# Kernel tuning notes

Measured on AMD Instinct MI355X. Metric: run time of the kernel, lower is better.

Reference implementation:

```python
import jax, jax.numpy as jnp
from jax import lax
import numpy as np

D_MODEL, D_INNER, D_STATE, DT_RANK, D_CONV = 1024, 2048, 16, 64, 4
BATCH, SEQ = 2, 1024
EPS = 1e-5


def setup_inputs() -> dict:
    key = jax.random.key(0)
    ks = jax.random.split(key, 10)
    s_in = 1.0 / np.sqrt(D_MODEL)
    s_x = 1.0 / np.sqrt(D_INNER)
    s_dt = DT_RANK ** -0.5
    # dt_proj bias init as in the source: inv-softplus of dt ~ logU(1e-3, 1e-1)
    dt = jnp.exp(jax.random.uniform(ks[7], (D_INNER,)) * (np.log(0.1) - np.log(0.001)) + np.log(0.001))
    dt = jnp.clip(dt, 1e-4, None)
    inv_dt = dt + jnp.log(-jnp.expm1(-dt))
    A_log = jnp.log(jnp.broadcast_to(jnp.arange(1, D_STATE + 1, dtype=jnp.float32), (D_INNER, D_STATE)))
    return {
        "u": jax.random.normal(ks[0], (BATCH, SEQ, D_MODEL), jnp.float32),
        "w_norm": jnp.ones((D_MODEL,), jnp.float32),
        "w_in": jax.random.normal(ks[1], (2 * D_INNER, D_MODEL), jnp.float32) * s_in,
        "conv_w": jax.random.normal(ks[2], (D_INNER, 1, D_CONV), jnp.float32) * 0.5,
        "conv_b": jax.random.normal(ks[3], (D_INNER,), jnp.float32) * 0.1,
        "w_x": jax.random.normal(ks[4], (DT_RANK + 2 * D_STATE, D_INNER), jnp.float32) * s_x,
        "w_dt": jax.random.uniform(ks[5], (D_INNER, DT_RANK), jnp.float32, -s_dt, s_dt),
        "b_dt": inv_dt,
        "A_log": A_log,
        "D_param": jnp.ones((D_INNER,), jnp.float32),
        "w_out": jax.random.normal(ks[6], (D_MODEL, D_INNER), jnp.float32) * s_x,
    }


def reference(u, w_norm, w_in, conv_w, conv_b, w_x, w_dt, b_dt, A_log, D_param, w_out):
    d_inner, d_state = A_log.shape
    dt_rank = w_dt.shape[1]
    # RMSNorm
    rms = jnp.sqrt(jnp.mean(u * u, axis=-1, keepdims=True) + EPS)
    u_norm = w_norm * (u / rms)
    # in_proj -> split x, z
    xz = jnp.einsum('bld,ed->ble', u_norm, w_in)
    x, z = jnp.split(xz, 2, axis=-1)
    # causal depthwise conv1d (left pad d_conv-1 == torch pad+truncate)
    xt = x.transpose(0, 2, 1)  # (B, D, L)
    conv = lax.conv_general_dilated(
        xt, conv_w, window_strides=(1,), padding=[(conv_w.shape[-1] - 1, 0)],
        feature_group_count=d_inner, dimension_numbers=('NCH', 'OIH', 'NCH'))
    x = jax.nn.silu((conv + conv_b[None, :, None]).transpose(0, 2, 1))  # (B, L, D)
    # x_proj -> dt, B, C
    xp = jnp.einsum('bld,ed->ble', x, w_x)
    dt_r = xp[..., :dt_rank]
    Bm = xp[..., dt_rank:dt_rank + d_state]   # (B, L, N)
    Cm = xp[..., dt_rank + d_state:]          # (B, L, N)
    dt = jax.nn.softplus(jnp.einsum('blr,dr->bld', dt_r, w_dt) + b_dt)
    # discretize
    A = -jnp.exp(A_log)                        # (D, N)
    dA = jnp.exp(dt[..., None] * A)            # (B, L, D, N)
    dBu = dt[..., None] * Bm[:, :, None, :] * x[..., None]  # (B, L, D, N)
    # sequential selective scan over L via lax.scan
    def step(s, inp):
        dA_t, dBu_t, C_t = inp
        s = dA_t * s + dBu_t                   # (B, D, N)
        y_t = jnp.einsum('bdn,bn->bd', s, C_t)
        return s, y_t
    s0 = jnp.zeros((u.shape[0], d_inner, d_state), x.dtype)
    _, ys = lax.scan(step, s0, (dA.transpose(1, 0, 2, 3), dBu.transpose(1, 0, 2, 3), Cm.transpose(1, 0, 2)))
    y = ys.transpose(1, 0, 2) + x * D_param    # (B, L, D)
    # gate + out_proj + residual
    y = y * jax.nn.silu(z)
    return jnp.einsum('bld,ed->ble', y, w_out) + u
```

## Files before the change

### kernel.cpp

```cpp
#include <hip/hip_runtime.h>
#include <hip/hip_bf16.h>
#include <cstdint>
#include <cstddef>

#define D_MODEL 1024
#define D_INNER 2048
#define D_STATE 16
#define DT_RANK 64
#define D_CONV  4
#define BATCH   2
#define SEQ     1024
#define NTOK    (BATCH*SEQ)
#define NC      32
#define CHUNK   (SEQ/NC)

typedef __bf16 bf16;
typedef __attribute__((ext_vector_type(8))) __bf16 bf16x8;
typedef __attribute__((ext_vector_type(4))) float f32x4;

#define WS_UNORM   0
#define WS_WIN     (WS_UNORM + 4194304)
#define WS_WOUT    (WS_WIN + 8388608)
#define WS_WDT     (WS_WOUT + 4194304)
#define WS_WX      (WS_WDT + 262144)
#define WS_DTR     (WS_WX + 524288)
#define WS_XZ      (WS_DTR + 262144)
#define WS_XC      (WS_XZ + 33554432)
#define WS_XCB     (WS_XC + 16777216)
#define WS_XP      (WS_XCB + 8388608)
#define WS_DT      (WS_XP + 1048576)
#define WS_P       (WS_DT + 16777216)
#define WS_Q       (WS_P + 8388608)
#define WS_S       (WS_Q + 8388608)
#define WS_YB      (WS_S + 8388608)

__device__ __forceinline__ void gload16(const void* gsrc, void* ldst) {
    __builtin_amdgcn_global_load_lds(
        (const __attribute__((address_space(1))) unsigned int*)gsrc,
        (__attribute__((address_space(3))) unsigned int*)ldst,
        16, 0, 0);
}

__global__ void mamba_cvt4(const float* __restrict__ s, bf16* __restrict__ d, int n4) {
    int i = blockIdx.x * 256 + threadIdx.x;
    if (i < n4) {
        float4 v = ((const float4*)s)[i];
        bf16* o = d + i * 4;
        o[0] = (bf16)v.x; o[1] = (bf16)v.y; o[2] = (bf16)v.z; o[3] = (bf16)v.w;
    }
}

__global__ void mamba_cvt_pad4(const float* __restrict__ s, bf16* __restrict__ d,
                               int nsrc4, int ntot4) {
    int i = blockIdx.x * 256 + threadIdx.x;
    if (i < ntot4) {
        bf16* o = d + i * 4;
        if (i < nsrc4) {
            float4 v = ((const float4*)s)[i];
            o[0] = (bf16)v.x; o[1] = (bf16)v.y; o[2] = (bf16)v.z; o[3] = (bf16)v.w;
        } else {
            o[0] = (bf16)0.f; o[1] = (bf16)0.f; o[2] = (bf16)0.f; o[3] = (bf16)0.f;
        }
    }
}

__global__ void mamba_dtr(const float* __restrict__ xp, bf16* __restrict__ dtr) {
    int i = blockIdx.x * 256 + threadIdx.x;
    int t = i >> 4, r4 = (i & 15) * 4;
    float4 v = *(const float4*)&xp[t * 128 + r4];
    bf16* o = dtr + t * 64 + r4;
    o[0] = (bf16)v.x; o[1] = (bf16)v.y; o[2] = (bf16)v.z; o[3] = (bf16)v.w;
}

__global__ void mamba_rmsnorm(const float* __restrict__ u, const float* __restrict__ w,
                              bf16* __restrict__ out) {
    int t = blockIdx.x;
    int tid = threadIdx.x;
    const float4 v = ((const float4*)(u + (size_t)t * D_MODEL))[tid];
    float ss = v.x * v.x + v.y * v.y + v.z * v.z + v.w * v.w;
    #pragma unroll
    for (int off = 32; off; off >>= 1) ss += __shfl_xor(ss, off, 64);
    __shared__ float red[4];
    int lane = tid & 63, wv = tid >> 6;
    if (lane == 0) red[wv] = ss;
    __syncthreads();
    float tot = red[0] + red[1] + red[2] + red[3];
    float rinv = rsqrtf(tot * (1.0f / D_MODEL) + 1e-5f);
    const float4 wn = ((const float4*)w)[tid];
    bf16* op = out + (size_t)t * D_MODEL + tid * 4;
    op[0] = (bf16)(v.x * wn.x * rinv);
    op[1] = (bf16)(v.y * wn.y * rinv);
    op[2] = (bf16)(v.z * wn.z * rinv);
    op[3] = (bf16)(v.w * wn.w * rinv);
}

template <int EPI, int SPLITK>
__global__ __launch_bounds__(256)
void mamba_gemm(const bf16* __restrict__ A, const bf16* __restrict__ B, float* __restrict__ C,
                int M, int N, int K, const float* __restrict__ aux) {
    __shared__ __align__(16) bf16 As[128 * 64];
    __shared__ __align__(16) bf16 Bs[128 * 64];
    int tid = threadIdx.x;
    int lane = tid & 63, w = tid >> 6;
    int wr = w >> 1, wc = w & 1;
    int m0 = blockIdx.y * 128, n0 = blockIdx.x * 128;
    int r16 = lane & 15, kq = lane >> 4;

    int Kc = K / SPLITK;
    int kbeg = blockIdx.z * Kc;
    int kend = kbeg + Kc;

    f32x4 acc[4][4];
    #pragma unroll
    for (int i = 0; i < 4; ++i)
        #pragma unroll
        for (int j = 0; j < 4; ++j)
            acc[i][j] = (f32x4){0.f, 0.f, 0.f, 0.f};

    int srow = tid >> 3;
    int p    = tid & 7;

    for (int k0 = kbeg; k0 < kend; k0 += 64) {
        __syncthreads();
        #pragma unroll
        for (int s = 0; s < 4; ++s) {
            int row = s * 32 + srow;
            int q = p ^ (row & 7);
            gload16(A + (size_t)(m0 + row) * K + k0 + q * 8,
                    (char*)As + s * 4096 + w * 1024);
            gload16(B + (size_t)(n0 + row) * K + k0 + q * 8,
                    (char*)Bs + s * 4096 + w * 1024);
        }
        __syncthreads();
        #pragma unroll
        for (int sub = 0; sub < 2; ++sub) {
            bf16x8 af[4], bfr[4];
            #pragma unroll
            for (int i = 0; i < 4; ++i) {
                int ra = wr * 64 + i * 16 + r16;
                int slot = (sub * 4 + kq) ^ (ra & 7);
                af[i] = *(const bf16x8*)((const char*)As + ra * 128 + slot * 16);
            }
            #pragma unroll
            for (int j = 0; j < 4; ++j) {
                int rb = wc * 64 + j * 16 + r16;
                int slot = (sub * 4 + kq) ^ (rb & 7);
                bfr[j] = *(const bf16x8*)((const char*)Bs + rb * 128 + slot * 16);
            }
            #pragma unroll
            for (int i = 0; i < 4; ++i)
                #pragma unroll
                for (int j = 0; j < 4; ++j)
                    acc[i][j] = __builtin_amdgcn_mfma_f32_16x16x32_bf16(af[i], bfr[j], acc[i][j], 0, 0, 0);
        }
    }

    #pragma unroll
    for (int i = 0; i < 4; ++i)
        #pragma unroll
        for (int j = 0; j < 4; ++j) {
            int col = n0 + wc * 64 + j * 16 + r16;
            #pragma unroll
            for (int r = 0; r < 4; ++r) {
                int row = m0 + wr * 64 + i * 16 + kq * 4 + r;
                float v = acc[i][j][r];
                size_t idx = (size_t)row * N + col;
                if (EPI == 1) {
                    v += aux[col];
                    v = (v > 20.f) ? v : log1pf(__expf(v));
                    C[idx] = v;
                } else if (EPI == 2) {
                    atomicAdd(&C[idx], v);
                } else {
                    C[idx] = v;
                }
            }
        }
}

__global__ void mamba_conv(const float* __restrict__ xz, const float* __restrict__ cw,
                           const float* __restrict__ cb, float* __restrict__ xc,
                           bf16* __restrict__ xcb) {
    int gid = blockIdx.x * 256 + threadIdx.x;
    int d = gid & (D_INNER - 1);
    int t = gid >> 11;
    int l = t & (SEQ - 1);
    int b = t >> 10;
    float acc = cb[d];
    #pragma unroll
    for (int j = 0; j < 4; ++j) {
        int li = l - 3 + j;
        if (li >= 0) acc += cw[d * 4 + j] * xz[(size_t)(b * SEQ + li) * 4096 + d];
    }
    float s = acc / (1.f + __expf(-acc));
    xc[gid] = s;
    xcb[gid] = (bf16)s;
}

__global__ void mamba_scan1(const float* __restrict__ dt, const float* __restrict__ xc,
                            const float* __restrict__ xp, const float* __restrict__ A_log,
                            float* __restrict__ P, float* __restrict__ Q) {
    int bid = blockIdx.x;
    int db = bid & 7, c = (bid >> 3) & 31, b = bid >> 8;
    int d = db * 256 + threadIdx.x;
    float a[D_STATE], pv[D_STATE], q[D_STATE];
    #pragma unroll
    for (int n = 0; n < D_STATE; ++n) {
        a[n] = -__expf(A_log[d * D_STATE + n]);
        pv[n] = 1.f; q[n] = 0.f;
    }
    int tbase = b * SEQ + c * CHUNK;
    for (int i = 0; i < CHUNK; ++i) {
        size_t t = tbase + i;
        float dtv = dt[t * D_INNER + d];
        float xv  = xc[t * D_INNER + d];
        float dtx = dtv * xv;
        const float* xpr = xp + t * 128;
        #pragma unroll
        for (int n = 0; n < D_STATE; ++n) {
            float e = __expf(dtv * a[n]);
            q[n] = e * q[n] + dtx * xpr[64 + n];
            pv[n] *= e;
        }
    }
    float* Pp = P + ((size_t)(b * D_INNER + d) * NC + c) * D_STATE;
    float* Qp = Q + ((size_t)(b * D_INNER + d) * NC + c) * D_STATE;
    #pragma unroll
    for (int n = 0; n < D_STATE; ++n) { Pp[n] = pv[n]; Qp[n] = q[n]; }
}

__global__ void mamba_scan2(const float* __restrict__ P, const float* __restrict__ Q,
                            float* __restrict__ S) {
    int gid = blockIdx.x * 256 + threadIdx.x;
    int bd = gid >> 4, n = gid & 15;
    size_t base = (size_t)bd * NC * D_STATE + n;
    float s = 0.f;
    for (int c = 0; c < NC; ++c) {
        S[base + c * D_STATE] = s;
        s = P[base + c * D_STATE] * s + Q[base + c * D_STATE];
    }
}

__global__ void mamba_scan3(const float* __restrict__ dt, const float* __restrict__ xc,
                            const float* __restrict__ xp, const float* __restrict__ A_log,
                            const float* __restrict__ S, const float* __restrict__ Dp,
                            const float* __restrict__ xz, bf16* __restrict__ yb) {
    int bid = blockIdx.x;
    int db = bid & 7, c = (bid >> 3) & 31, b = bid >> 8;
    int d = db * 256 + threadIdx.x;
    float a[D_STATE], s[D_STATE];
    const float* Sp = S + ((size_t)(b * D_INNER + d) * NC + c) * D_STATE;
    #pragma unroll
    for (int n = 0; n < D_STATE; ++n) {
        a[n] = -__expf(A_log[d * D_STATE + n]);
        s[n] = Sp[n];
    }
    float Dpd = Dp[d];
    int tbase = b * SEQ + c * CHUNK;
    for (int i = 0; i < CHUNK; ++i) {
        size_t t = tbase + i;
        float dtv = dt[t * D_INNER + d];
        float xv  = xc[t * D_INNER + d];
        float dtx = dtv * xv;
        const float* xpr = xp + t * 128;
        float y = 0.f;
        #pragma unroll
        for (int n = 0; n < D_STATE; ++n) {
            float e = __expf(dtv * a[n]);
            s[n] = e * s[n] + dtx * xpr[64 + n];
            y += s[n] * xpr[80 + n];
        }
        float zv = xz[t * 4096 + 2048 + d];
        float sig = 1.f / (1.f + __expf(-zv));
        float out = (y + xv * Dpd) * (zv * sig);
        yb[t * D_INNER + d] = (bf16)out;
    }
}

extern "C" void kernel_launch(void* const* d_in, const int* in_sizes, int n_in,
                              void* d_out, int out_size, void* d_ws, size_t ws_size,
                              hipStream_t stream) {
    const float* u      = (const float*)d_in[0];
    const float* w_norm = (const float*)d_in[1];
    const float* w_in   = (const float*)d_in[2];
    const float* conv_w = (const float*)d_in[3];
    const float* conv_b = (const float*)d_in[4];
    const float* w_x    = (const float*)d_in[5];
    const float* w_dt   = (const float*)d_in[6];
    const float* b_dt   = (const float*)d_in[7];
    const float* A_log  = (const float*)d_in[8];
    const float* D_par  = (const float*)d_in[9];
    const float* w_out  = (const float*)d_in[10];
    float* out = (float*)d_out;

    char* ws = (char*)d_ws;
    bf16* unorm = (bf16*)(ws + WS_UNORM);
    bf16* winb  = (bf16*)(ws + WS_WIN);
    bf16* woutb = (bf16*)(ws + WS_WOUT);
    bf16* wdtb  = (bf16*)(ws + WS_WDT);
    bf16* wxb   = (bf16*)(ws + WS_WX);
    bf16* dtrb  = (bf16*)(ws + WS_DTR);
    float* xz   = (float*)(ws + WS_XZ);
    float* xc   = (float*)(ws + WS_XC);
    bf16* xcb   = (bf16*)(ws + WS_XCB);
    float* xp   = (float*)(ws + WS_XP);
    float* dtb  = (float*)(ws + WS_DT);
    float* Pb   = (float*)(ws + WS_P);
    float* Qb   = (float*)(ws + WS_Q);
    float* Sb   = (float*)(ws + WS_S);
    bf16* yb    = (bf16*)(ws + WS_YB);

    mamba_cvt4<<<4096, 256, 0, stream>>>(w_in, winb, 2 * D_INNER * D_MODEL / 4);
    mamba_cvt4<<<2048, 256, 0, stream>>>(w_out, woutb, D_MODEL * D_INNER / 4);
    mamba_cvt4<<<128, 256, 0, stream>>>(w_dt, wdtb, D_INNER * DT_RANK / 4);
    mamba_cvt_pad4<<<256, 256, 0, stream>>>(w_x, wxb, (DT_RANK + 2 * D_STATE) * D_INNER / 4,
                                            128 * D_INNER / 4);

    mamba_rmsnorm<<<NTOK, 256, 0, stream>>>(u, w_norm, unorm);

    mamba_gemm<0, 1><<<dim3(32, 16, 1), 256, 0, stream>>>(unorm, winb, xz,
                                                          NTOK, 2 * D_INNER, D_MODEL, nullptr);

    mamba_conv<<<NTOK * D_INNER / 256, 256, 0, stream>>>(xz, conv_w, conv_b, xc, xcb);

    hipMemsetAsync(xp, 0, (size_t)NTOK * 128 * 4, stream);
    mamba_gemm<2, 8><<<dim3(1, 16, 8), 256, 0, stream>>>(xcb, wxb, xp,
                                                         NTOK, 128, D_INNER, nullptr);

    mamba_dtr<<<128, 256, 0, stream>>>(xp, dtrb);

    mamba_gemm<1, 1><<<dim3(16, 16, 1), 256, 0, stream>>>(dtrb, wdtb, dtb,
                                                          NTOK, D_INNER, DT_RANK, b_dt);

    mamba_scan1<<<512, 256, 0, stream>>>(dtb, xc, xp, A_log, Pb, Qb);
    mamba_scan2<<<256, 256, 0, stream>>>(Pb, Qb, Sb);
    mamba_scan3<<<512, 256, 0, stream>>>(dtb, xc, xp, A_log, Sb, D_par, xz, yb);

    hipMemcpyAsync(out, u, (size_t)NTOK * D_MODEL * 4, hipMemcpyDeviceToDevice, stream);
    mamba_gemm<2, 4><<<dim3(8, 16, 4), 256, 0, stream>>>(yb, woutb, out,
                                                         NTOK, D_MODEL, D_INNER, nullptr);
}
```

Before: 294.1 us.

## Fuse prep kernels, store activations in bf16, and fuse dt conversion into dt GEMM

Merges the weight conversions, RMSNorm, residual copy and xp memset into one multi-role launch. The in_proj output xz and the conv output are now stored only in bf16, which halves their memory traffic and drops the fp32 xc buffer. A dedicated dt GEMM reads the fp32 xp and w_dt directly and converts them while loading into shared memory, which removes the dtr and w_dt conversion kernels. The cost is lower precision for x and z in the scan and gate, plus fewer separate launches.

New measurement: 273.9 us. 1.07x faster.

```diff
diff --git a/kernel.cpp b/kernel.cpp
--- a/kernel.cpp
+++ b/kernel.cpp
@@ -21,12 +21,9 @@
 #define WS_UNORM   0
 #define WS_WIN     (WS_UNORM + 4194304)
 #define WS_WOUT    (WS_WIN + 8388608)
-#define WS_WDT     (WS_WOUT + 4194304)
-#define WS_WX      (WS_WDT + 262144)
-#define WS_DTR     (WS_WX + 524288)
-#define WS_XZ      (WS_DTR + 262144)
-#define WS_XC      (WS_XZ + 33554432)
-#define WS_XCB     (WS_XC + 16777216)
+#define WS_WX      (WS_WOUT + 4194304)
+#define WS_XZB     (WS_WX + 524288)
+#define WS_XCB     (WS_XZB + 16777216)
 #define WS_XP      (WS_XCB + 8388608)
 #define WS_DT      (WS_XP + 1048576)
 #define WS_P       (WS_DT + 16777216)
@@ -41,63 +38,63 @@
         16, 0, 0);
 }
 
-__global__ void mamba_cvt4(const float* __restrict__ s, bf16* __restrict__ d, int n4) {
-    int i = blockIdx.x * 256 + threadIdx.x;
-    if (i < n4) {
-        float4 v = ((const float4*)s)[i];
-        bf16* o = d + i * 4;
+__global__ void mamba_prep(const float* __restrict__ u, const float* __restrict__ w_norm,
+                           const float* __restrict__ w_in, const float* __restrict__ w_x,
+                           const float* __restrict__ w_out,
+                           bf16* __restrict__ unorm, bf16* __restrict__ winb,
+                           bf16* __restrict__ wxb, bf16* __restrict__ woutb,
+                           float* __restrict__ outp, float* __restrict__ xp) {
+    __shared__ float red[4];
+    int bid = blockIdx.x, tid = threadIdx.x;
+    if (bid < 2048) {
+        int t = bid;
+        const float4 v = ((const float4*)(u + (size_t)t * D_MODEL))[tid];
+        float ss = v.x * v.x + v.y * v.y + v.z * v.z + v.w * v.w;
+        #pragma unroll
+        for (int off = 32; off; off >>= 1) ss += __shfl_xor(ss, off, 64);
+        int lane = tid & 63, wv = tid >> 6;
+        if (lane == 0) red[wv] = ss;
+        __syncthreads();
+        float tot = red[0] + red[1] + red[2] + red[3];
+        float rinv = rsqrtf(tot * (1.0f / D_MODEL) + 1e-5f);
+        const float4 wn = ((const float4*)w_norm)[tid];
+        bf16* op = unorm + (size_t)t * D_MODEL + tid * 4;
+        op[0] = (bf16)(v.x * wn.x * rinv);
+        op[1] = (bf16)(v.y * wn.y * rinv);
+        op[2] = (bf16)(v.z * wn.z * rinv);
+        op[3] = (bf16)(v.w * wn.w * rinv);
+    } else if (bid < 6144) {
+        int i = (bid - 2048) * 256 + tid;
+        float4 v = ((const float4*)w_in)[i];
+        bf16* o = winb + i * 4;
         o[0] = (bf16)v.x; o[1] = (bf16)v.y; o[2] = (bf16)v.z; o[3] = (bf16)v.w;
-    }
-}
-
-__global__ void mamba_cvt_pad4(const float* __restrict__ s, bf16* __restrict__ d,
-                               int nsrc4, int ntot4) {
-    int i = blockIdx.x * 256 + threadIdx.x;
-    if (i < ntot4) {
-        bf16* o = d + i * 4;
-        if (i < nsrc4) {
-            float4 v = ((const float4*)s)[i];
+    } else if (bid < 8192) {
+        int i = (bid - 6144) * 256 + tid;
+        float4 v = ((const float4*)w_out)[i];
+        bf16* o = woutb + i * 4;
+        o[0] = (bf16)v.x; o[1] = (bf16)v.y; o[2] = (bf16)v.z; o[3] = (bf16)v.w;
+    } else if (bid < 8448) {
+        int i = (bid - 8192) * 256 + tid;
+        bf16* o = wxb + i * 4;
+        if (i < 49152) {
+            float4 v = ((const float4*)w_x)[i];
             o[0] = (bf16)v.x; o[1] = (bf16)v.y; o[2] = (bf16)v.z; o[3] = (bf16)v.w;
         } else {
             o[0] = (bf16)0.f; o[1] = (bf16)0.f; o[2] = (bf16)0.f; o[3] = (bf16)0.f;
         }
-    }
-}
-
-__global__ void mamba_dtr(const float* __restrict__ xp, bf16* __restrict__ dtr) {
-    int i = blockIdx.x * 256 + threadIdx.x;
-    int t = i >> 4, r4 = (i & 15) * 4;
-    float4 v = *(const float4*)&xp[t * 128 + r4];
-    bf16* o = dtr + t * 64 + r4;
-    o[0] = (bf16)v.x; o[1] = (bf16)v.y; o[2] = (bf16)v.z; o[3] = (bf16)v.w;
-}
-
-__global__ void mamba_rmsnorm(const float* __restrict__ u, const float* __restrict__ w,
-                              bf16* __restrict__ out) {
-    int t = blockIdx.x;
-    int tid = threadIdx.x;
-    const float4 v = ((const float4*)(u + (size_t)t * D_MODEL))[tid];
-    float ss = v.x * v.x + v.y * v.y + v.z * v.z + v.w * v.w;
-    #pragma unroll
-    for (int off = 32; off; off >>= 1) ss += __shfl_xor(ss, off, 64);
-    __shared__ float red[4];
-    int lane = tid & 63, wv = tid >> 6;
-    if (lane == 0) red[wv] = ss;
-    __syncthreads();
-    float tot = red[0] + red[1] + red[2] + red[3];
-    float rinv = rsqrtf(tot * (1.0f / D_MODEL) + 1e-5f);
-    const float4 wn = ((const float4*)w)[tid];
-    bf16* op = out + (size_t)t * D_MODEL + tid * 4;
-    op[0] = (bf16)(v.x * wn.x * rinv);
-    op[1] = (bf16)(v.y * wn.y * rinv);
-    op[2] = (bf16)(v.z * wn.z * rinv);
-    op[3] = (bf16)(v.w * wn.w * rinv);
+    } else if (bid < 10496) {
+        int i = (bid - 8448) * 256 + tid;
+        ((float4*)outp)[i] = ((const float4*)u)[i];
+    } else {
+        int i = (bid - 10496) * 256 + tid;
+        ((float4*)xp)[i] = (float4){0.f, 0.f, 0.f, 0.f};
+    }
 }
 
 template <int EPI, int SPLITK>
 __global__ __launch_bounds__(256)
-void mamba_gemm(const bf16* __restrict__ A, const bf16* __restrict__ B, float* __restrict__ C,
-                int M, int N, int K, const float* __restrict__ aux) {
+void mamba_gemm(const bf16* __restrict__ A, const bf16* __restrict__ B, void* __restrict__ Cv,
+                int M, int N, int K) {
     __shared__ __align__(16) bf16 As[128 * 64];
     __shared__ __align__(16) bf16 Bs[128 * 64];
     int tid = threadIdx.x;
@@ -165,39 +162,110 @@
                 int row = m0 + wr * 64 + i * 16 + kq * 4 + r;
                 float v = acc[i][j][r];
                 size_t idx = (size_t)row * N + col;
-                if (EPI == 1) {
-                    v += aux[col];
-                    v = (v > 20.f) ? v : log1pf(__expf(v));
-                    C[idx] = v;
-                } else if (EPI == 2) {
-                    atomicAdd(&C[idx], v);
+                if (EPI == 2) {
+                    atomicAdd(&((float*)Cv)[idx], v);
                 } else {
-                    C[idx] = v;
+                    ((bf16*)Cv)[idx] = (bf16)v;
                 }
             }
         }
 }
 
-__global__ void mamba_conv(const float* __restrict__ xz, const float* __restrict__ cw,
-                           const float* __restrict__ cb, float* __restrict__ xc,
-                           bf16* __restrict__ xcb) {
+__global__ __launch_bounds__(256)
+void mamba_dtgemm(const float* __restrict__ xp, const float* __restrict__ wdt,
+                  const float* __restrict__ bdt, float* __restrict__ dt) {
+    __shared__ __align__(16) bf16 As[128 * 64];
+    __shared__ __align__(16) bf16 Bs[128 * 64];
+    int tid = threadIdx.x;
+    int lane = tid & 63, w = tid >> 6;
+    int wr = w >> 1, wc = w & 1;
+    int m0 = blockIdx.y * 128, n0 = blockIdx.x * 128;
+    int r16 = lane & 15, kq = lane >> 4;
+
+    #pragma unroll
+    for (int s4 = 0; s4 < 4; ++s4) {
+        int s = s4 * 256 + tid;
+        int row = s >> 3, p = s & 7;
+        int ps = p ^ (row & 7);
+        const float* ga = xp + (size_t)(m0 + row) * 128 + p * 8;
+        const float* gb = wdt + (size_t)(n0 + row) * 64 + p * 8;
+        float4 a0 = *(const float4*)ga, a1 = *(const float4*)(ga + 4);
+        float4 b0 = *(const float4*)gb, b1 = *(const float4*)(gb + 4);
+        bf16x8 av, bv;
+        av[0] = (bf16)a0.x; av[1] = (bf16)a0.y; av[2] = (bf16)a0.z; av[3] = (bf16)a0.w;
+        av[4] = (bf16)a1.x; av[5] = (bf16)a1.y; av[6] = (bf16)a1.z; av[7] = (bf16)a1.w;
+        bv[0] = (bf16)b0.x; bv[1] = (bf16)b0.y; bv[2] = (bf16)b0.z; bv[3] = (bf16)b0.w;
+        bv[4] = (bf16)b1.x; bv[5] = (bf16)b1.y; bv[6] = (bf16)b1.z; bv[7] = (bf16)b1.w;
+        *(bf16x8*)((char*)As + row * 128 + ps * 16) = av;
+        *(bf16x8*)((char*)Bs + row * 128 + ps * 16) = bv;
+    }
+    __syncthreads();
+
+    f32x4 acc[4][4];
+    #pragma unroll
+    for (int i = 0; i < 4; ++i)
+        #pragma unroll
+        for (int j = 0; j < 4; ++j)
+            acc[i][j] = (f32x4){0.f, 0.f, 0.f, 0.f};
+
+    #pragma unroll
+    for (int sub = 0; sub < 2; ++sub) {
+        bf16x8 af[4], bfr[4];
+        #pragma unroll
+        for (int i = 0; i < 4; ++i) {
+            int ra = wr * 64 + i * 16 + r16;
+            int slot = (sub * 4 + kq) ^ (ra & 7);
+            af[i] = *(const bf16x8*)((const char*)As + ra * 128 + slot * 16);
+        }
+        #pragma unroll
+        for (int j = 0; j < 4; ++j) {
+            int rb = wc * 64 + j * 16 + r16;
+            int slot = (sub * 4 + kq) ^ (rb & 7);
+            bfr[j] = *(const bf16x8*)((const char*)Bs + rb * 128 + slot * 16);
+        }
+        #pragma unroll
+        for (int i = 0; i < 4; ++i)
+            #pragma unroll
+            for (int j = 0; j < 4; ++j)
+                acc[i][j] = __builtin_amdgcn_mfma_f32_16x16x32_bf16(af[i], bfr[j], acc[i][j], 0, 0, 0);
+    }
+
+    #pragma unroll
+    for (int i = 0; i < 4; ++i)
+        #pragma unroll
+        for (int j = 0; j < 4; ++j) {
+            int col = n0 + wc * 64 + j * 16 + r16;
+            float bias = bdt[col];
+            #pragma unroll
+            for (int r = 0; r < 4; ++r) {
+                int row = m0 + wr * 64 + i * 16 + kq * 4 + r;
+                float v = acc[i][j][r] + bias;
+                v = (v > 20.f) ? v : log1pf(__expf(v));
+                dt[(size_t)row * D_INNER + col] = v;
+            }
+        }
+}
+
+__global__ void mamba_conv(const bf16* __restrict__ xzb, const float* __restrict__ cw,
+                           const float* __restrict__ cb, bf16* __restrict__ xcb) {
     int gid = blockIdx.x * 256 + threadIdx.x;
     int d = gid & (D_INNER - 1);
     int t = gid >> 11;
     int l = t & (SEQ - 1);
     int b = t >> 10;
+    float4 wv = ((const float4*)cw)[d];
+    const float wj[4] = {wv.x, wv.y, wv.z, wv.w};
     float acc = cb[d];
     #pragma unroll
     for (int j = 0; j < 4; ++j) {
         int li = l - 3 + j;
-        if (li >= 0) acc += cw[d * 4 + j] * xz[(size_t)(b * SEQ + li) * 4096 + d];
+        if (li >= 0) acc += wj[j] * (float)xzb[(size_t)(b * SEQ + li) * 4096 + d];
     }
     float s = acc / (1.f + __expf(-acc));
-    xc[gid] = s;
     xcb[gid] = (bf16)s;
 }
 
-__global__ void mamba_scan1(const float* __restrict__ dt, const float* __restrict__ xc,
+__global__ void mamba_scan1(const float* __restrict__ dt, const bf16* __restrict__ xcb,
                             const float* __restrict__ xp, const float* __restrict__ A_log,
                             float* __restrict__ P, float* __restrict__ Q) {
     int bid = blockIdx.x;
@@ -213,7 +281,7 @@
     for (int i = 0; i < CHUNK; ++i) {
         size_t t = tbase + i;
         float dtv = dt[t * D_INNER + d];
-        float xv  = xc[t * D_INNER + d];
+        float xv  = (float)xcb[t * D_INNER + d];
         float dtx = dtv * xv;
         const float* xpr = xp + t * 128;
         #pragma unroll
@@ -241,10 +309,10 @@
     }
 }
 
-__global__ void mamba_scan3(const float* __restrict__ dt, const float* __restrict__ xc,
+__global__ void mamba_scan3(const float* __restrict__ dt, const bf16* __restrict__ xcb,
                             const float* __restrict__ xp, const float* __restrict__ A_log,
                             const float* __restrict__ S, const float* __restrict__ Dp,
-                            const float* __restrict__ xz, bf16* __restrict__ yb) {
+                            const bf16* __restrict__ xzb, bf16* __restrict__ yb) {
     int bid = blockIdx.x;
     int db = bid & 7, c = (bid >> 3) & 31, b = bid >> 8;
     int d = db * 256 + threadIdx.x;
@@ -260,7 +328,7 @@
     for (int i = 0; i < CHUNK; ++i) {
         size_t t = tbase + i;
         float dtv = dt[t * D_INNER + d];
-        float xv  = xc[t * D_INNER + d];
+        float xv  = (float)xcb[t * D_INNER + d];
         float dtx = dtv * xv;
         const float* xpr = xp + t * 128;
         float y = 0.f;
@@ -270,7 +338,7 @@
             s[n] = e * s[n] + dtx * xpr[64 + n];
             y += s[n] * xpr[80 + n];
         }
-        float zv = xz[t * 4096 + 2048 + d];
+        float zv = (float)xzb[t * 4096 + 2048 + d];
         float sig = 1.f / (1.f + __expf(-zv));
         float out = (y + xv * Dpd) * (zv * sig);
         yb[t * D_INNER + d] = (bf16)out;
@@ -297,11 +365,8 @@
     bf16* unorm = (bf16*)(ws + WS_UNORM);
     bf16* winb  = (bf16*)(ws + WS_WIN);
     bf16* woutb = (bf16*)(ws + WS_WOUT);
-    bf16* wdtb  = (bf16*)(ws + WS_WDT);
     bf16* wxb   = (bf16*)(ws + WS_WX);
-    bf16* dtrb  = (bf16*)(ws + WS_DTR);
-    float* xz   = (float*)(ws + WS_XZ);
-    float* xc   = (float*)(ws + WS_XC);
+    bf16* xzb   = (bf16*)(ws + WS_XZB);
     bf16* xcb   = (bf16*)(ws + WS_XCB);
     float* xp   = (float*)(ws + WS_XP);
     float* dtb  = (float*)(ws + WS_DT);
@@ -310,33 +375,23 @@
     float* Sb   = (float*)(ws + WS_S);
     bf16* yb    = (bf16*)(ws + WS_YB);
 
-    mamba_cvt4<<<4096, 256, 0, stream>>>(w_in, winb, 2 * D_INNER * D_MODEL / 4);
-    mamba_cvt4<<<2048, 256, 0, stream>>>(w_out, woutb, D_MODEL * D_INNER / 4);
-    mamba_cvt4<<<128, 256, 0, stream>>>(w_dt, wdtb, D_INNER * DT_RANK / 4);
-    mamba_cvt_pad4<<<256, 256, 0, stream>>>(w_x, wxb, (DT_RANK + 2 * D_STATE) * D_INNER / 4,
-                                            128 * D_INNER / 4);
-
-    mamba_rmsnorm<<<NTOK, 256, 0, stream>>>(u, w_norm, unorm);
-
-    mamba_gemm<0, 1><<<dim3(32, 16, 1), 256, 0, stream>>>(unorm, winb, xz,
-                                                          NTOK, 2 * D_INNER, D_MODEL, nullptr);
-
-    mamba_conv<<<NTOK * D_INNER / 256, 256, 0, stream>>>(xz, conv_w, conv_b, xc, xcb);
-
-    hipMemsetAsync(xp, 0, (size_t)NTOK * 128 * 4, stream);
+    mamba_prep<<<10752, 256, 0, stream>>>(u, w_norm, w_in, w_x, w_out,
+                                          unorm, winb, wxb, woutb, out, xp);
+
+    mamba_gemm<3, 1><<<dim3(32, 16, 1), 256, 0, stream>>>(unorm, winb, xzb,
+                                                          NTOK, 2 * D_INNER, D_MODEL);
+
+    mamba_conv<<<NTOK * D_INNER / 256, 256, 0, stream>>>(xzb, conv_w, conv_b, xcb);
+
     mamba_gemm<2, 8><<<dim3(1, 16, 8), 256, 0, stream>>>(xcb, wxb, xp,
-                                                         NTOK, 128, D_INNER, nullptr);
-
-    mamba_dtr<<<128, 256, 0, stream>>>(xp, dtrb);
-
-    mamba_gemm<1, 1><<<dim3(16, 16, 1), 256, 0, stream>>>(dtrb, wdtb, dtb,
-                                                          NTOK, D_INNER, DT_RANK, b_dt);
-
-    mamba_scan1<<<512, 256, 0, stream>>>(dtb, xc, xp, A_log, Pb, Qb);
+                                                         NTOK, 128, D_INNER);
+
+    mamba_dtgemm<<<dim3(16, 16), 256, 0, stream>>>(xp, w_dt, b_dt, dtb);
+
+    mamba_scan1<<<512, 256, 0, stream>>>(dtb, xcb, xp, A_log, Pb, Qb);
     mamba_scan2<<<256, 256, 0, stream>>>(Pb, Qb, Sb);
-    mamba_scan3<<<512, 256, 0, stream>>>(dtb, xc, xp, A_log, Sb, D_par, xz, yb);
-
-    hipMemcpyAsync(out, u, (size_t)NTOK * D_MODEL * 4, hipMemcpyDeviceToDevice, stream);
+    mamba_scan3<<<512, 256, 0, stream>>>(dtb, xcb, xp, A_log, Sb, D_par, xzb, yb);
+
     mamba_gemm<2, 4><<<dim3(8, 16, 4), 256, 0, stream>>>(yb, woutb, out,
-                                                         NTOK, D_MODEL, D_INNER, nullptr);
-}
+                                                         NTOK, D_MODEL, D_INNER);
+}
```
